# Kernel tuning notes

Measured on AMD Instinct MI355X. Metric: run time of the kernel, lower is better.

Reference implementation:

```python
import jax, jax.numpy as jnp
import numpy as np

C, CP, H, D, N, B = 128, 16, 8, 16, 2048, 1
INF = 1e8


def _ln(x, w=None, b=None, eps=1e-5):
    mu = jnp.mean(x, axis=-1, keepdims=True)
    var = jnp.var(x, axis=-1, keepdims=True)
    y = (x - mu) * jax.lax.rsqrt(var + eps)
    if w is not None:
        y = y * w
    if b is not None:
        y = y + b
    return y


def _ada_ln(a, s, sln_w, gw, gb, skw):
    # AdaLN: non-affine LN on a, weight-only LN on s, sigmoid gate + skip from s
    a = _ln(a)
    s = _ln(s, sln_w)
    return jax.nn.sigmoid(s @ gw + gb) * a + s @ skw


def _betas(n, n_keys=128, inf=INF):
    # centers at 16 + 32k; query row i belongs to window i//32, keys within +/- n_keys//2 of center
    i = jnp.arange(n)
    c = 16 + 32 * (i // 32)
    j = jnp.arange(n)
    ok = (j[None, :] >= (c - n_keys // 2)[:, None]) & (j[None, :] < (c + n_keys // 2)[:, None])
    return jnp.where(ok, 0.0, -inf).astype(jnp.float32)


def _forward(atom_single, atom_proj, atom_pair, mask,
             a_sln_w, a_gate_w, a_gate_b, a_skip_w,
             wq, bq, wk, wv, wg, bg, wo, bo,
             lnz_w, lnz_b, wz, wog, bog,
             t_sln_w, t_gate_w, t_gate_b, t_skip_w,
             w_sw, w_hid, w_out, t_wog, t_bog):
    bs, n, _ = atom_single.shape
    betas = _betas(n)
    # ---- AttentionPairBias (input_gating=True, residual handled outside) ----
    a = _ada_ln(atom_single, atom_proj, a_sln_w, a_gate_w, a_gate_b, a_skip_w)
    q = (a @ wq + bq).reshape(bs, n, H, D)
    k = (a @ wk).reshape(bs, n, H, D)
    v = (a @ wv).reshape(bs, n, H, D)
    pair_bias = _ln(atom_pair, lnz_w, lnz_b) @ wz            # (bs, n, n, H)
    pair_bias = jnp.transpose(pair_bias, (0, 3, 1, 2)) + betas  # (bs, H, n, n)
    mask_bias = (INF * (mask - 1.0))[:, None, None, :]          # (bs, 1, 1, n)
    logits = jnp.einsum('bqhd,bkhd->bhqk', q, k) / np.float32(np.sqrt(D))
    logits = logits + pair_bias + mask_bias
    probs = jax.nn.softmax(logits, axis=-1)
    o = jnp.einsum('bhqk,bkhd->bqhd', probs, v)
    g = jax.nn.sigmoid(a @ wg + bg).reshape(bs, n, H, D)
    o = (o * g).reshape(bs, n, H * D) @ wo + bo
    o = jax.nn.sigmoid(atom_proj @ wog + bog) * o             # conditioned output gate
    atom_single = atom_single + o
    # ---- ConditionedTransitionBlock (SwiGLU, n=2) ----
    t = _ada_ln(atom_single, atom_proj, t_sln_w, t_gate_w, t_gate_b, t_skip_w)
    hidden = jax.nn.silu(t @ w_sw) * (t @ w_hid)              # (bs, n, 2C)
    t_out = jax.nn.sigmoid(atom_proj @ t_wog + t_bog) * (hidden @ w_out)
    return atom_single + t_out


def setup_inputs() -> dict:
    key = jax.random.key(0)
    ks = iter(jax.random.split(key, 40))
    rn = lambda shape, s=1.0: jax.random.normal(next(ks), shape, jnp.float32) * s
    p = 0.05
    return {
        "atom_single": rn((B, N, C)),
        "atom_proj": rn((B, N, C)),
        "atom_pair": rn((B, N, N, CP)),
        "mask": jnp.ones((B, N), jnp.float32),
        "a_sln_w": jnp.ones((C,), jnp.float32), "a_gate_w": rn((C, C), p), "a_gate_b": jnp.zeros((C,), jnp.float32), "a_skip_w": rn((C, C), p),
        "wq": rn((C, C), p), "bq": jnp.zeros((C,), jnp.float32),
        "wk": rn((C, C), p), "wv": rn((C, C), p),
        "wg": rn((C, C), p), "bg": jnp.ones((C,), jnp.float32),
        "wo": rn((C, C), p), "bo": jnp.zeros((C,), jnp.float32),
        "lnz_w": jnp.ones((CP,), jnp.float32), "lnz_b": jnp.zeros((CP,), jnp.float32), "wz": rn((CP, H), p),
        "wog": rn((C, C), p), "bog": jnp.full((C,), -2.0, jnp.float32),
        "t_sln_w": jnp.ones((C,), jnp.float32), "t_gate_w": rn((C, C), p), "t_gate_b": jnp.zeros((C,), jnp.float32), "t_skip_w": rn((C, C), p),
        "w_sw": rn((C, 2 * C), p), "w_hid": rn((C, 2 * C), p), "w_out": rn((2 * C, C), p),
        "t_wog": rn((C, C), p), "t_bog": jnp.full((C,), -2.0, jnp.float32),
    }


def reference(atom_single, atom_proj, atom_pair, mask,
              a_sln_w, a_gate_w, a_gate_b, a_skip_w,
              wq, bq, wk, wv, wg, bg, wo, bo,
              lnz_w, lnz_b, wz, wog, bog,
              t_sln_w, t_gate_w, t_gate_b, t_skip_w,
              w_sw, w_hid, w_out, t_wog, t_bog):
    out = _forward(atom_single, atom_proj, atom_pair, mask,
                   a_sln_w, a_gate_w, a_gate_b, a_skip_w,
                   wq, bq, wk, wv, wg, bg, wo, bo,
                   lnz_w, lnz_b, wz, wog, bog,
                   t_sln_w, t_gate_w, t_gate_b, t_skip_w,
                   w_sw, w_hid, w_out, t_wog, t_bog)
    return (out, atom_proj, atom_pair)
```

## Files before the change

### kernel.cpp

```cpp
#include <hip/hip_runtime.h>
#include <math.h>

#define NN 2048
#define CC 128
#define HH 8
#define DD 16
#define NKEY 128
#define INFV 1e8f
#define NPR ((long)NN * CC / 4)
#define NCPTOT (NPR + (long)NN * NN * 4)
#define SLOT 2176
#define ANP 36
#define ASLOT 1152

__device__ __forceinline__ float sigm(float x) { return 1.f / (1.f + expf(-x)); }

struct Args {
  const float *atom_single, *atom_proj, *atom_pair, *mask;
  const float *a_sln_w, *a_gate_w, *a_gate_b, *a_skip_w;
  const float *wq, *bq, *wk, *wv, *wg, *bg, *wo, *bo;
  const float *lnz_w, *lnz_b, *wz, *wog, *bog;
  const float *t_sln_w, *t_gate_w, *t_gate_b, *t_skip_w;
  const float *w_sw, *w_hid, *w_out, *t_wog, *t_bog;
  float *out;
  float *s_ln_a, *s_ln_t, *ln_as, *a_mat, *qm, *km, *vm, *gm, *ogm,
        *single2, *t_mat, *hidden, *bias;
  long cut[9];
};

__device__ __forceinline__ void copy_span(const Args& a, int s, long rb, long nb, int tid) {
  long c0 = a.cut[s], c1 = a.cut[s + 1];
  const float4* proj4 = (const float4*)a.atom_proj;
  const float4* pair4 = (const float4*)a.atom_pair;
  float4* dst = (float4*)(a.out + (long)NN * CC);
  long stride = nb * 256;
  long i = c0 + rb * 256 + tid;
  for (; i + 3 * stride < c1; i += 4 * stride) {
    long i1 = i + stride, i2 = i + 2 * stride, i3 = i + 3 * stride;
    float4 x0 = (i  < NPR) ? proj4[i]  : pair4[i  - NPR];
    float4 x1 = (i1 < NPR) ? proj4[i1] : pair4[i1 - NPR];
    float4 x2 = (i2 < NPR) ? proj4[i2] : pair4[i2 - NPR];
    float4 x3 = (i3 < NPR) ? proj4[i3] : pair4[i3 - NPR];
    dst[i] = x0; dst[i1] = x1; dst[i2] = x2; dst[i3] = x3;
  }
  for (; i < c1; i += stride) dst[i] = (i < NPR) ? proj4[i] : pair4[i - NPR];
}

__device__ __forceinline__ void gsingle_pf(float* sm, int tid,
    const float* __restrict__ A1, const float* __restrict__ B1, int lda1, int ldb1, int K1,
    int r0, int c0, float acc1[4][4]) {
  float* buf0 = sm;
  float* buf1 = sm + 2 * SLOT;
  int tr = (tid >> 4) * 4, tc = (tid & 15) * 4;
  int ar = tid >> 5, ak = tid & 31;
  int bk = tid >> 6, bc = tid & 63;
  float pA[2][8], pB[2][8];
  auto LD = [&](int kb, int s) {
#pragma unroll
    for (int j = 0; j < 8; ++j) {
      pA[s][j] = A1[(long)(r0 + ar + 8 * j) * lda1 + kb + ak];
      pB[s][j] = B1[(long)(kb + bk + 4 * j) * ldb1 + c0 + bc];
    }
  };
  auto WR = [&](float* buf, int s) {
    float* B1s_ = buf + SLOT;
#pragma unroll
    for (int j = 0; j < 8; ++j) {
      buf[ak * 68 + ar + 8 * j] = pA[s][j];
      B1s_[(bk + 4 * j) * 68 + bc] = pB[s][j];
    }
  };
  auto CMP = [&](float* cur) {
    float* As_ = cur;
    float* B1s_ = cur + SLOT;
#pragma unroll 4
    for (int k = 0; k < 32; ++k) {
      float4 a1 = *(const float4*)&As_[k * 68 + tr];
      float4 b1 = *(const float4*)&B1s_[k * 68 + tc];
      float a1v[4] = {a1.x, a1.y, a1.z, a1.w};
      float b1v[4] = {b1.x, b1.y, b1.z, b1.w};
#pragma unroll
      for (int i = 0; i < 4; ++i)
#pragma unroll
        for (int j = 0; j < 4; ++j) acc1[i][j] = fmaf(a1v[i], b1v[j], acc1[i][j]);
    }
  };
  int nk = K1 / 32;
  LD(0, 0);
  if (nk > 1) LD(32, 1);
  WR(buf0, 0);
  __syncthreads();
  for (int kt = 0; kt < nk; kt += 2) {
    if (kt + 2 < nk) LD((kt + 2) * 32, 0);
    if (kt + 1 < nk) WR(buf1, 1);
    CMP(buf0);
    __syncthreads();
    if (kt + 1 >= nk) break;
    if (kt + 3 < nk) LD((kt + 3) * 32, 1);
    if (kt + 2 < nk) WR(buf0, 0);
    CMP(buf1);
    __syncthreads();
  }
}

template <bool SHA>
__device__ __forceinline__ void gdual32(float* sm, int tid,
    const float* __restrict__ A1, const float* __restrict__ B1, int lda1, int ldb1, int K1,
    const float* __restrict__ A2, const float* __restrict__ B2, int lda2, int ldb2, int K2,
    int r0, int c0, float acc1[2][4], float acc2[2][4]) {
  const int offB1 = ASLOT;
  const int offA2 = ASLOT + SLOT;
  const int offB2 = SHA ? (ASLOT + SLOT) : (2 * ASLOT + SLOT);
  const int bufsz = SHA ? (ASLOT + 2 * SLOT) : (2 * ASLOT + 2 * SLOT);
  float* buf0 = sm;
  float* buf1 = sm + bufsz;
  int tr2 = (tid >> 4) * 2, tc4 = (tid & 15) * 4;
  int ar = tid & 31, ak4 = (tid >> 5) * 4;
  int bk = tid >> 6, bc = tid & 63;
  float4 vA1[2], vA2[2];
  float pB1[2][8], pB2[2][8];

  auto LD = [&](int kb, int s, bool twof) {
    vA1[s] = *(const float4*)&A1[(long)(r0 + ar) * lda1 + kb + ak4];
#pragma unroll
    for (int j = 0; j < 8; ++j)
      pB1[s][j] = B1[(long)(kb + bk + 4 * j) * ldb1 + c0 + bc];
    if (twof) {
      if constexpr (!SHA) vA2[s] = *(const float4*)&A2[(long)(r0 + ar) * lda2 + kb + ak4];
#pragma unroll
      for (int j = 0; j < 8; ++j)
        pB2[s][j] = B2[(long)(kb + bk + 4 * j) * ldb2 + c0 + bc];
    }
  };
  auto WR = [&](float* buf, int s, bool twof) {
    float* As_ = buf;
    float* B1s_ = buf + offB1;
    As_[(ak4 + 0) * ANP + ar] = vA1[s].x;
    As_[(ak4 + 1) * ANP + ar] = vA1[s].y;
    As_[(ak4 + 2) * ANP + ar] = vA1[s].z;
    As_[(ak4 + 3) * ANP + ar] = vA1[s].w;
#pragma unroll
    for (int j = 0; j < 8; ++j) B1s_[(bk + 4 * j) * 68 + bc] = pB1[s][j];
    if (twof) {
      float* B2s_ = buf + offB2;
      if constexpr (!SHA) {
        float* A2s_ = buf + offA2;
        A2s_[(ak4 + 0) * ANP + ar] = vA2[s].x;
        A2s_[(ak4 + 1) * ANP + ar] = vA2[s].y;
        A2s_[(ak4 + 2) * ANP + ar] = vA2[s].z;
        A2s_[(ak4 + 3) * ANP + ar] = vA2[s].w;
      }
#pragma unroll
      for (int j = 0; j < 8; ++j) B2s_[(bk + 4 * j) * 68 + bc] = pB2[s][j];
    }
  };
  auto CMP = [&](float* cur, bool twoc) {
    float* As_ = cur;
    float* B1s_ = cur + offB1;
    float* A2s_ = cur + offA2;
    float* B2s_ = cur + offB2;
    if (twoc) {
#pragma unroll 4
      for (int k = 0; k < 32; ++k) {
        float2 a1 = *(const float2*)&As_[k * ANP + tr2];
        float4 b1 = *(const float4*)&B1s_[k * 68 + tc4];
        float4 b2 = *(const float4*)&B2s_[k * 68 + tc4];
        float2 a2;
        if constexpr (SHA) a2 = a1; else a2 = *(const float2*)&A2s_[k * ANP + tr2];
        float a1v[2] = {a1.x, a1.y};
        float a2v[2] = {a2.x, a2.y};
        float b1v[4] = {b1.x, b1.y, b1.z, b1.w};
        float b2v[4] = {b2.x, b2.y, b2.z, b2.w};
#pragma unroll
        for (int i = 0; i < 2; ++i)
#pragma unroll
          for (int j = 0; j < 4; ++j) {
            acc1[i][j] = fmaf(a1v[i], b1v[j], acc1[i][j]);
            acc2[i][j] = fmaf(a2v[i], b2v[j], acc2[i][j]);
          }
      }
    } else {
#pragma unroll 4
      for (int k = 0; k < 32; ++k) {
        float2 a1 = *(const float2*)&As_[k * ANP + tr2];
        float4 b1 = *(const float4*)&B1s_[k * 68 + tc4];
        float a1v[2] = {a1.x, a1.y};
        float b1v[4] = {b1.x, b1.y, b1.z, b1.w};
#pragma unroll
        for (int i = 0; i < 2; ++i)
#pragma unroll
          for (int j = 0; j < 4; ++j) acc1[i][j] = fmaf(a1v[i], b1v[j], acc1[i][j]);
      }
    }
  };

  int nk = K1 / 32;
  LD(0, 0, 0 < K2);
  if (nk > 1) LD(32, 1, 32 < K2);
  WR(buf0, 0, 0 < K2);
  __syncthreads();
  for (int kt = 0; kt < nk; kt += 2) {
    if (kt + 2 < nk) LD((kt + 2) * 32, 0, (kt + 2) * 32 < K2);
    if (kt + 1 < nk) WR(buf1, 1, (kt + 1) * 32 < K2);
    CMP(buf0, kt * 32 < K2);
    __syncthreads();
    if (kt + 1 >= nk) break;
    if (kt + 3 < nk) LD((kt + 3) * 32, 1, (kt + 3) * 32 < K2);
    if (kt + 2 < nk) WR(buf0, 0, (kt + 2) * 32 < K2);
    CMP(buf1, (kt + 1) * 32 < K2);
    __syncthreads();
  }
}

__device__ __forceinline__ void bias_stage(const Args& a, long lo, long hi,
                                           int bid, int nb, int tid, float* sm) {
  float* swz = sm;
  float* swn = sm + 128;
  float* sbn = sm + 144;
  if (tid < 128) swz[tid] = a.wz[tid];
  else if (tid < 144) swn[tid - 128] = a.lnz_w[tid - 128];
  else if (tid < 160) sbn[tid - 144] = a.lnz_b[tid - 144];
  __syncthreads();
  for (long e = lo + bid * 256 + tid; e < hi; e += (long)nb * 256) {
    int q = (int)(e >> 7), kk = (int)(e & 127);
    int k = (q >> 5) * 32 - 48 + kk;
    float o[HH];
    if (k >= 0 && k < NN) {
      const float4* p = (const float4*)(a.atom_pair + ((long)q * NN + k) * 16);
      float4 x0 = p[0], x1 = p[1], x2 = p[2], x3 = p[3];
      float x[16] = {x0.x, x0.y, x0.z, x0.w, x1.x, x1.y, x1.z, x1.w,
                     x2.x, x2.y, x2.z, x2.w, x3.x, x3.y, x3.z, x3.w};
      float s = 0.f, ss = 0.f;
#pragma unroll
      for (int c = 0; c < 16; ++c) { s += x[c]; ss += x[c] * x[c]; }
      float mu = s * (1.f / 16.f);
      float r = rsqrtf(ss * (1.f / 16.f) - mu * mu + 1e-5f);
#pragma unroll
      for (int h = 0; h < HH; ++h) o[h] = 0.f;
#pragma unroll
      for (int c = 0; c < 16; ++c) {
        float y = (x[c] - mu) * r * swn[c] + sbn[c];
#pragma unroll
        for (int h = 0; h < HH; ++h) o[h] = fmaf(y, swz[c * HH + h], o[h]);
      }
      float mb = INFV * (a.mask[k] - 1.f);
#pragma unroll
      for (int h = 0; h < HH; ++h) o[h] += mb;
    } else {
#pragma unroll
      for (int h = 0; h < HH; ++h) o[h] = -INFV;
    }
#pragma unroll
    for (int h = 0; h < HH; ++h) a.bias[(long)h * NN * NKEY + e] = o[h];
  }
}

__device__ __forceinline__ void ln1_stage(const Args& a, int lb, int tid) {
  int base = lb * 64;
  int lane = tid & 63;
  for (int r = base + (tid >> 6); r < base + 64; r += 4) {
    {
      float2 v = *(const float2*)(a.atom_single + (long)r * CC + lane * 2);
      float s = v.x + v.y, ss = v.x * v.x + v.y * v.y;
#pragma unroll
      for (int m = 1; m < 64; m <<= 1) { s += __shfl_xor(s, m); ss += __shfl_xor(ss, m); }
      float mu = s * (1.f / CC);
      float rr = rsqrtf(ss * (1.f / CC) - mu * mu + 1e-5f);
      *(float2*)(a.ln_as + (long)r * CC + lane * 2) =
          make_float2((v.x - mu) * rr, (v.y - mu) * rr);
    }
    {
      float2 v = *(const float2*)(a.atom_proj + (long)r * CC + lane * 2);
      float s = v.x + v.y, ss = v.x * v.x + v.y * v.y;
#pragma unroll
      for (int m = 1; m < 64; m <<= 1) { s += __shfl_xor(s, m); ss += __shfl_xor(ss, m); }
      float mu = s * (1.f / CC);
      float rr = rsqrtf(ss * (1.f / CC) - mu * mu + 1e-5f);
      float y0 = (v.x - mu) * rr, y1 = (v.y - mu) * rr;
      float2 wa = *(const float2*)(a.a_sln_w + lane * 2);
      float2 wt = *(const float2*)(a.t_sln_w + lane * 2);
      *(float2*)(a.s_ln_a + (long)r * CC + lane * 2) = make_float2(y0 * wa.x, y1 * wa.y);
      *(float2*)(a.s_ln_t + (long)r * CC + lane * 2) = make_float2(y0 * wt.x, y1 * wt.y);
    }
  }
}

template <bool INLN>
__device__ __forceinline__ void adaln32_stage(const Args& a, const float* A, const float* gw,
                                              const float* gb, const float* skw,
                                              const float* lnm_or_src, float* outp,
                                              int bid, int tid, float* sm, float* sst) {
  int r0 = (bid & 63) * 32, c0 = (bid >> 6) * 64;
  if constexpr (INLN) {
    int row = tid >> 3, cg = (tid & 7) * 16;
    const float* src = lnm_or_src + (long)(r0 + row) * CC + cg;
    float s = 0.f, ss = 0.f;
#pragma unroll
    for (int j = 0; j < 4; ++j) {
      float4 v = *(const float4*)(src + j * 4);
      s += v.x + v.y + v.z + v.w;
      ss += v.x * v.x + v.y * v.y + v.z * v.z + v.w * v.w;
    }
#pragma unroll
    for (int m = 1; m < 8; m <<= 1) { s += __shfl_xor(s, m); ss += __shfl_xor(ss, m); }
    if ((tid & 7) == 0) {
      float mu = s * (1.f / CC);
      sst[2 * row] = mu;
      sst[2 * row + 1] = rsqrtf(ss * (1.f / CC) - mu * mu + 1e-5f);
    }
  }
  float acc1[2][4] = {{0}}, acc2[2][4] = {{0}};
  gdual32<true>(sm, tid, A, gw, 128, 128, 128, A, skw, 128, 128, 128, r0, c0, acc1, acc2);
  int tr2 = (tid >> 4) * 2, tc4 = (tid & 15) * 4;
#pragma unroll
  for (int i = 0; i < 2; ++i) {
    long r = r0 + tr2 + i;
    float lv[4];
    if constexpr (INLN) {
      float mu = sst[2 * (tr2 + i)], rr = sst[2 * (tr2 + i) + 1];
      float4 sv = *(const float4*)(lnm_or_src + r * CC + c0 + tc4);
      lv[0] = (sv.x - mu) * rr; lv[1] = (sv.y - mu) * rr;
      lv[2] = (sv.z - mu) * rr; lv[3] = (sv.w - mu) * rr;
    } else {
      float4 lm = *(const float4*)(lnm_or_src + r * CC + c0 + tc4);
      lv[0] = lm.x; lv[1] = lm.y; lv[2] = lm.z; lv[3] = lm.w;
    }
    float o[4];
#pragma unroll
    for (int j = 0; j < 4; ++j)
      o[j] = sigm(acc1[i][j] + gb[c0 + tc4 + j]) * lv[j] + acc2[i][j];
    *(float4*)(outp + r * CC + c0 + tc4) = make_float4(o[0], o[1], o[2], o[3]);
  }
}

__device__ __forceinline__ void gemm4_stage(const Args& a, int bid, int tid, float* sm) {
  int r0 = (bid & 31) * 64;
  int cg4 = (bid >> 5) * 64;
  int mat = cg4 >> 7;
  int c0 = cg4 & 127;
  const float* B = (mat == 0) ? a.wq : (mat == 1) ? a.wk : (mat == 2) ? a.wv : a.wg;
  float acc[4][4] = {{0}};
  gsingle_pf(sm, tid, a.a_mat, B, 128, 128, 128, r0, c0, acc);
  float* outp = (mat == 0) ? a.qm : (mat == 1) ? a.km : (mat == 2) ? a.vm : a.gm;
  int tr = (tid >> 4) * 4, tc = (tid & 15) * 4;
#pragma unroll
  for (int i = 0; i < 4; ++i) {
    long r = r0 + tr + i;
    float o[4];
#pragma unroll
    for (int j = 0; j < 4; ++j) {
      float x = acc[i][j];
      if (mat == 0) x += a.bq[c0 + tc + j];
      if (mat == 3) x = sigm(x + a.bg[c0 + tc + j]);
      o[j] = x;
    }
    *(float4*)(outp + r * CC + c0 + tc) = make_float4(o[0], o[1], o[2], o[3]);
  }
}

__device__ __forceinline__ void attn_unit(const Args& a, int u, int tid, float* sm) {
  int w = u & 63, h = u >> 6;
  int q0 = w * 32, k0 = w * 32 - 48;
  float* Qs = sm;
  float* Ks = sm + 544;
  float* Vs = sm + 3104;
  float* Ps = sm + 5664;
  for (int i = tid; i < 32 * 16; i += 256) {
    int qi = i >> 4, d = i & 15;
    Qs[qi * 17 + d] = a.qm[(long)(q0 + qi) * CC + h * DD + d];
  }
  for (int i = tid; i < 128 * 16; i += 256) {
    int kk = i >> 4, d = i & 15;
    int k = k0 + kk;
    bool ok = (k >= 0 && k < NN);
    Ks[kk * 20 + d] = ok ? a.km[(long)k * CC + h * DD + d] : 0.f;
    Vs[kk * 20 + d] = ok ? a.vm[(long)k * CC + h * DD + d] : 0.f;
  }
  __syncthreads();
  int qi = tid >> 3, kg = tid & 7;
  const float* brow = a.bias + (long)h * NN * NKEY + (long)(q0 + qi) * NKEY;
  float qreg[16];
#pragma unroll
  for (int d = 0; d < 16; ++d) qreg[d] = Qs[qi * 17 + d];
  float l[16];
#pragma unroll
  for (int j = 0; j < 16; ++j) {
    int kk = kg + 8 * j;
    const float4* kr = (const float4*)&Ks[kk * 20];
    float4 k0v = kr[0], k1v = kr[1], k2v = kr[2], k3v = kr[3];
    float acc = 0.f;
    acc = fmaf(qreg[0], k0v.x, acc);  acc = fmaf(qreg[1], k0v.y, acc);
    acc = fmaf(qreg[2], k0v.z, acc);  acc = fmaf(qreg[3], k0v.w, acc);
    acc = fmaf(qreg[4], k1v.x, acc);  acc = fmaf(qreg[5], k1v.y, acc);
    acc = fmaf(qreg[6], k1v.z, acc);  acc = fmaf(qreg[7], k1v.w, acc);
    acc = fmaf(qreg[8], k2v.x, acc);  acc = fmaf(qreg[9], k2v.y, acc);
    acc = fmaf(qreg[10], k2v.z, acc); acc = fmaf(qreg[11], k2v.w, acc);
    acc = fmaf(qreg[12], k3v.x, acc); acc = fmaf(qreg[13], k3v.y, acc);
    acc = fmaf(qreg[14], k3v.z, acc); acc = fmaf(qreg[15], k3v.w, acc);
    l[j] = acc * 0.25f + brow[kk];
  }
  float m = l[0];
#pragma unroll
  for (int j = 1; j < 16; ++j) m = fmaxf(m, l[j]);
#pragma unroll
  for (int mm = 1; mm < 8; mm <<= 1) m = fmaxf(m, __shfl_xor(m, mm));
  float sum = 0.f;
#pragma unroll
  for (int j = 0; j < 16; ++j) { l[j] = expf(l[j] - m); sum += l[j]; }
#pragma unroll
  for (int mm = 1; mm < 8; mm <<= 1) sum += __shfl_xor(sum, mm);
  float inv = 1.f / sum;
#pragma unroll
  for (int j = 0; j < 16; ++j) Ps[qi * 132 + kg + 8 * j] = l[j] * inv;
  __syncthreads();
  int d0 = tid & 7;
  float o0 = 0.f, o1 = 0.f;
#pragma unroll 8
  for (int kk = 0; kk < 128; ++kk) {
    float p = Ps[qi * 132 + kk];
    o0 = fmaf(p, Vs[kk * 20 + d0], o0);
    o1 = fmaf(p, Vs[kk * 20 + d0 + 8], o1);
  }
  long base = (long)(q0 + qi) * CC + h * DD;
  a.ogm[base + d0] = o0 * a.gm[base + d0];
  a.ogm[base + d0 + 8] = o1 * a.gm[base + d0 + 8];
}

__device__ __forceinline__ void out1_32(const Args& a, int bid, int tid, float* sm) {
  int r0 = (bid & 63) * 32, c0 = (bid >> 6) * 64;
  float accX[2][4] = {{0}}, accW[2][4] = {{0}};
  gdual32<false>(sm, tid, a.ogm, a.wo, 128, 128, 128, a.atom_proj, a.wog, 128, 128, 128,
                 r0, c0, accX, accW);
  int tr2 = (tid >> 4) * 2, tc4 = (tid & 15) * 4;
#pragma unroll
  for (int i = 0; i < 2; ++i) {
    long r = r0 + tr2 + i;
    float4 sv = *(const float4*)(a.atom_single + r * CC + c0 + tc4);
    float s[4] = {sv.x, sv.y, sv.z, sv.w};
    float o[4];
#pragma unroll
    for (int j = 0; j < 4; ++j) {
      int c = c0 + tc4 + j;
      o[j] = s[j] + sigm(accW[i][j] + a.bog[c]) * (accX[i][j] + a.bo[c]);
    }
    *(float4*)(a.single2 + r * CC + c0 + tc4) = make_float4(o[0], o[1], o[2], o[3]);
  }
}

__device__ __forceinline__ void swiglu_32(const Args& a, int bid, int tid, float* sm) {
  int r0 = (bid & 63) * 32, c0 = (bid >> 6) * 64;
  float acc1[2][4] = {{0}}, acc2[2][4] = {{0}};
  gdual32<true>(sm, tid, a.t_mat, a.w_sw, 128, 256, 128, a.t_mat, a.w_hid, 128, 256, 128,
                r0, c0, acc1, acc2);
  int tr2 = (tid >> 4) * 2, tc4 = (tid & 15) * 4;
#pragma unroll
  for (int i = 0; i < 2; ++i) {
    long r = r0 + tr2 + i;
    float o[4];
#pragma unroll
    for (int j = 0; j < 4; ++j) {
      float x = acc1[i][j];
      o[j] = x * sigm(x) * acc2[i][j];
    }
    *(float4*)(a.hidden + r * 256 + c0 + tc4) = make_float4(o[0], o[1], o[2], o[3]);
  }
}

__device__ __forceinline__ void out2_32(const Args& a, int bid, int tid, float* sm) {
  int r0 = (bid & 63) * 32, c0 = (bid >> 6) * 64;
  float accX[2][4] = {{0}}, accW[2][4] = {{0}};
  gdual32<false>(sm, tid, a.hidden, a.w_out, 256, 128, 256, a.atom_proj, a.t_wog, 128, 128, 128,
                 r0, c0, accX, accW);
  int tr2 = (tid >> 4) * 2, tc4 = (tid & 15) * 4;
#pragma unroll
  for (int i = 0; i < 2; ++i) {
    long r = r0 + tr2 + i;
    float4 sv = *(const float4*)(a.single2 + r * CC + c0 + tc4);
    float s[4] = {sv.x, sv.y, sv.z, sv.w};
    float o[4];
#pragma unroll
    for (int j = 0; j < 4; ++j) {
      int c = c0 + tc4 + j;
      o[j] = s[j] + sigm(accW[i][j] + a.t_bog[c]) * accX[i][j];
    }
    *(float4*)(a.out + r * CC + c0 + tc4) = make_float4(o[0], o[1], o[2], o[3]);
  }
}

#define BIAS_TOT ((long)NN * NKEY)
#define BIAS_1 (BIAS_TOT / 3)
#define BIAS_2 (2 * BIAS_TOT / 3)

__global__ __launch_bounds__(256) void k_head(Args a) {
  __shared__ __align__(16) float sm[160];
  int bid = blockIdx.x, tid = threadIdx.x;
  if (bid < 96) bias_stage(a, 0, BIAS_1, bid, 96, tid, sm);
  else if (bid < 128) ln1_stage(a, bid - 96, tid);
  else copy_span(a, 0, bid - 128, gridDim.x - 128, tid);
}

__global__ __launch_bounds__(256) void k_adaln_a(Args a) {
  __shared__ __align__(16) float sm[2 * (ASLOT + 2 * SLOT) + 64];
  int bid = blockIdx.x, tid = threadIdx.x;
  if (bid < 128)
    adaln32_stage<false>(a, a.s_ln_a, a.a_gate_w, a.a_gate_b, a.a_skip_w, a.ln_as, a.a_mat,
                         bid, tid, sm, nullptr);
  else if (bid < 224) bias_stage(a, BIAS_1, BIAS_2, bid - 128, 96, tid, sm);
  else copy_span(a, 1, bid - 224, gridDim.x - 224, tid);
}

__global__ __launch_bounds__(256) void k_qkvg(Args a) {
  __shared__ __align__(16) float sm[2 * 2 * SLOT];
  int bid = blockIdx.x, tid = threadIdx.x;
  if (bid < 256) gemm4_stage(a, bid, tid, sm);
  else if (bid < 352) bias_stage(a, BIAS_2, BIAS_TOT, bid - 256, 96, tid, sm);
  else copy_span(a, 2, bid - 352, gridDim.x - 352, tid);
}

__global__ __launch_bounds__(256) void k_attn(Args a) {
  __shared__ __align__(16) float sm[9888];
  int bid = blockIdx.x, tid = threadIdx.x;
  if (bid < 512) attn_unit(a, bid, tid, sm);
  else copy_span(a, 3, bid - 512, gridDim.x - 512, tid);
}

__global__ __launch_bounds__(256) void k_out1(Args a) {
  __shared__ __align__(16) float sm[2 * (2 * ASLOT + 2 * SLOT)];
  int bid = blockIdx.x, tid = threadIdx.x;
  if (bid < 128) out1_32(a, bid, tid, sm);
  else copy_span(a, 4, bid - 128, gridDim.x - 128, tid);
}

__global__ __launch_bounds__(256) void k_adaln_t(Args a) {
  __shared__ __align__(16) float sm[2 * (ASLOT + 2 * SLOT) + 64];
  int bid = blockIdx.x, tid = threadIdx.x;
  if (bid < 128)
    adaln32_stage<true>(a, a.s_ln_t, a.t_gate_w, a.t_gate_b, a.t_skip_w, a.single2, a.t_mat,
                        bid, tid, sm, sm + 2 * (ASLOT + 2 * SLOT));
  else copy_span(a, 5, bid - 128, gridDim.x - 128, tid);
}

__global__ __launch_bounds__(256) void k_swiglu(Args a) {
  __shared__ __align__(16) float sm[2 * (ASLOT + 2 * SLOT)];
  int bid = blockIdx.x, tid = threadIdx.x;
  if (bid < 256) swiglu_32(a, bid, tid, sm);
  else copy_span(a, 6, bid - 256, gridDim.x - 256, tid);
}

__global__ __launch_bounds__(256) void k_out2(Args a) {
  __shared__ __align__(16) float sm[2 * (2 * ASLOT + 2 * SLOT)];
  int bid = blockIdx.x, tid = threadIdx.x;
  if (bid < 128) out2_32(a, bid, tid, sm);
  else copy_span(a, 7, bid - 128, gridDim.x - 128, tid);
}

extern "C" void kernel_launch(void* const* d_in, const int* in_sizes, int n_in,
                              void* d_out, int out_size, void* d_ws, size_t ws_size,
                              hipStream_t stream) {
  (void)in_sizes; (void)n_in; (void)out_size; (void)ws_size;
  Args a;
  a.atom_single = (const float*)d_in[0];
  a.atom_proj   = (const float*)d_in[1];
  a.atom_pair   = (const float*)d_in[2];
  a.mask        = (const float*)d_in[3];
  a.a_sln_w  = (const float*)d_in[4];
  a.a_gate_w = (const float*)d_in[5];
  a.a_gate_b = (const float*)d_in[6];
  a.a_skip_w = (const float*)d_in[7];
  a.wq = (const float*)d_in[8];  a.bq = (const float*)d_in[9];
  a.wk = (const float*)d_in[10]; a.wv = (const float*)d_in[11];
  a.wg = (const float*)d_in[12]; a.bg = (const float*)d_in[13];
  a.wo = (const float*)d_in[14]; a.bo = (const float*)d_in[15];
  a.lnz_w = (const float*)d_in[16]; a.lnz_b = (const float*)d_in[17];
  a.wz = (const float*)d_in[18];
  a.wog = (const float*)d_in[19]; a.bog = (const float*)d_in[20];
  a.t_sln_w  = (const float*)d_in[21];
  a.t_gate_w = (const float*)d_in[22];
  a.t_gate_b = (const float*)d_in[23];
  a.t_skip_w = (const float*)d_in[24];
  a.w_sw  = (const float*)d_in[25];
  a.w_hid = (const float*)d_in[26];
  a.w_out = (const float*)d_in[27];
  a.t_wog = (const float*)d_in[28];
  a.t_bog = (const float*)d_in[29];
  a.out = (float*)d_out;

  float* ws = (float*)d_ws;
  const long NC = (long)NN * CC;
  a.s_ln_a  = ws + 0 * NC;
  a.s_ln_t  = ws + 1 * NC;
  a.ln_as   = ws + 2 * NC;
  a.a_mat   = ws + 3 * NC;
  a.qm      = ws + 4 * NC;
  a.km      = ws + 5 * NC;
  a.vm      = ws + 6 * NC;
  a.gm      = ws + 7 * NC;
  a.ogm     = ws + 8 * NC;
  a.single2 = ws + 9 * NC;
  a.t_mat   = ws + 11 * NC;
  a.hidden  = ws + 12 * NC;
  a.bias    = ws + 14 * NC;

  const int cum[9] = {0, 9, 17, 24, 32, 40, 48, 56, 64};
  for (int i = 0; i < 9; ++i) a.cut[i] = NCPTOT * (long)cum[i] / 64;

  k_head   <<<2048, 256, 0, stream>>>(a);
  k_adaln_a<<<2048, 256, 0, stream>>>(a);
  k_qkvg   <<<2048, 256, 0, stream>>>(a);
  k_attn   <<<2048, 256, 0, stream>>>(a);
  k_out1   <<<2048, 256, 0, stream>>>(a);
  k_adaln_t<<<2048, 256, 0, stream>>>(a);
  k_swiglu <<<2048, 256, 0, stream>>>(a);
  k_out2   <<<2048, 256, 0, stream>>>(a);
}
```

Before: 156.7 us.

## Use atomic work-stealing for passthrough copies and nontemporal loads/stores

The passthrough copy of atom_proj and atom_pair into the output was statically split across leftover blocks in each stage kernel. Now every block, including compute blocks once they finish their stage work, takes chunks of the copy from a per-stage atomic counter, so copy work follows whichever blocks free up. The copy also uses nontemporal loads and stores to keep streaming data out of the caches. The cost is atomic traffic and extra barriers per chunk. There is also a counter-reset ordering risk: counters are zeroed in k_head and first used in the next kernel, which the stream ordering covers.

```diff
diff --git a/kernel.cpp b/kernel.cpp
--- a/kernel.cpp
+++ b/kernel.cpp
@@ -12,6 +12,9 @@
 #define SLOT 2176
 #define ANP 36
 #define ASLOT 1152
+#define CHUNK4 2048L
+
+typedef float f4 __attribute__((ext_vector_type(4)));
 
 __device__ __forceinline__ float sigm(float x) { return 1.f / (1.f + expf(-x)); }
 
@@ -25,25 +28,59 @@
   float *out;
   float *s_ln_a, *s_ln_t, *ln_as, *a_mat, *qm, *km, *vm, *gm, *ogm,
         *single2, *t_mat, *hidden, *bias;
+  unsigned* cnt;
   long cut[9];
 };
 
 __device__ __forceinline__ void copy_span(const Args& a, int s, long rb, long nb, int tid) {
   long c0 = a.cut[s], c1 = a.cut[s + 1];
-  const float4* proj4 = (const float4*)a.atom_proj;
-  const float4* pair4 = (const float4*)a.atom_pair;
-  float4* dst = (float4*)(a.out + (long)NN * CC);
+  const f4* proj4 = (const f4*)a.atom_proj;
+  const f4* pair4 = (const f4*)a.atom_pair;
+  f4* dst = (f4*)(a.out + (long)NN * CC);
   long stride = nb * 256;
   long i = c0 + rb * 256 + tid;
   for (; i + 3 * stride < c1; i += 4 * stride) {
     long i1 = i + stride, i2 = i + 2 * stride, i3 = i + 3 * stride;
-    float4 x0 = (i  < NPR) ? proj4[i]  : pair4[i  - NPR];
-    float4 x1 = (i1 < NPR) ? proj4[i1] : pair4[i1 - NPR];
-    float4 x2 = (i2 < NPR) ? proj4[i2] : pair4[i2 - NPR];
-    float4 x3 = (i3 < NPR) ? proj4[i3] : pair4[i3 - NPR];
-    dst[i] = x0; dst[i1] = x1; dst[i2] = x2; dst[i3] = x3;
-  }
-  for (; i < c1; i += stride) dst[i] = (i < NPR) ? proj4[i] : pair4[i - NPR];
+    f4 x0 = (i  < NPR) ? __builtin_nontemporal_load(&proj4[i])
+                       : __builtin_nontemporal_load(&pair4[i - NPR]);
+    f4 x1 = (i1 < NPR) ? __builtin_nontemporal_load(&proj4[i1])
+                       : __builtin_nontemporal_load(&pair4[i1 - NPR]);
+    f4 x2 = (i2 < NPR) ? __builtin_nontemporal_load(&proj4[i2])
+                       : __builtin_nontemporal_load(&pair4[i2 - NPR]);
+    f4 x3 = (i3 < NPR) ? __builtin_nontemporal_load(&proj4[i3])
+                       : __builtin_nontemporal_load(&pair4[i3 - NPR]);
+    __builtin_nontemporal_store(x0, &dst[i]);
+    __builtin_nontemporal_store(x1, &dst[i1]);
+    __builtin_nontemporal_store(x2, &dst[i2]);
+    __builtin_nontemporal_store(x3, &dst[i3]);
+  }
+  for (; i < c1; i += stride) {
+    f4 v = (i < NPR) ? __builtin_nontemporal_load(&proj4[i])
+                     : __builtin_nontemporal_load(&pair4[i - NPR]);
+    __builtin_nontemporal_store(v, &dst[i]);
+  }
+}
+
+__device__ void copy_steal(const Args& a, int s, int tid) {
+  __shared__ unsigned sticket;
+  long c0 = a.cut[s], c1 = a.cut[s + 1];
+  const f4* proj4 = (const f4*)a.atom_proj;
+  const f4* pair4 = (const f4*)a.atom_pair;
+  f4* dst = (f4*)(a.out + (long)NN * CC);
+  unsigned* cnt = a.cnt + s;
+  while (true) {
+    __syncthreads();
+    if (tid == 0) sticket = atomicAdd(cnt, 1u);
+    __syncthreads();
+    long base = c0 + (long)sticket * CHUNK4;
+    if (base >= c1) break;
+    long end = (base + CHUNK4 < c1) ? base + CHUNK4 : c1;
+    for (long i = base + tid; i < end; i += 256) {
+      f4 v = (i < NPR) ? __builtin_nontemporal_load(&proj4[i])
+                       : __builtin_nontemporal_load(&pair4[i - NPR]);
+      __builtin_nontemporal_store(v, &dst[i]);
+    }
+  }
 }
 
 __device__ __forceinline__ void gsingle_pf(float* sm, int tid,
@@ -494,6 +531,7 @@
 __global__ __launch_bounds__(256) void k_head(Args a) {
   __shared__ __align__(16) float sm[160];
   int bid = blockIdx.x, tid = threadIdx.x;
+  if (bid == 0 && tid < 8) a.cnt[tid] = 0;
   if (bid < 96) bias_stage(a, 0, BIAS_1, bid, 96, tid, sm);
   else if (bid < 128) ln1_stage(a, bid - 96, tid);
   else copy_span(a, 0, bid - 128, gridDim.x - 128, tid);
@@ -506,7 +544,7 @@
     adaln32_stage<false>(a, a.s_ln_a, a.a_gate_w, a.a_gate_b, a.a_skip_w, a.ln_as, a.a_mat,
                          bid, tid, sm, nullptr);
   else if (bid < 224) bias_stage(a, BIAS_1, BIAS_2, bid - 128, 96, tid, sm);
-  else copy_span(a, 1, bid - 224, gridDim.x - 224, tid);
+  copy_steal(a, 1, tid);
 }
 
 __global__ __launch_bounds__(256) void k_qkvg(Args a) {
@@ -514,21 +552,21 @@
   int bid = blockIdx.x, tid = threadIdx.x;
   if (bid < 256) gemm4_stage(a, bid, tid, sm);
   else if (bid < 352) bias_stage(a, BIAS_2, BIAS_TOT, bid - 256, 96, tid, sm);
-  else copy_span(a, 2, bid - 352, gridDim.x - 352, tid);
+  copy_steal(a, 2, tid);
 }
 
 __global__ __launch_bounds__(256) void k_attn(Args a) {
   __shared__ __align__(16) float sm[9888];
   int bid = blockIdx.x, tid = threadIdx.x;
   if (bid < 512) attn_unit(a, bid, tid, sm);
-  else copy_span(a, 3, bid - 512, gridDim.x - 512, tid);
+  copy_steal(a, 3, tid);
 }
 
 __global__ __launch_bounds__(256) void k_out1(Args a) {
   __shared__ __align__(16) float sm[2 * (2 * ASLOT + 2 * SLOT)];
   int bid = blockIdx.x, tid = threadIdx.x;
   if (bid < 128) out1_32(a, bid, tid, sm);
-  else copy_span(a, 4, bid - 128, gridDim.x - 128, tid);
+  copy_steal(a, 4, tid);
 }
 
 __global__ __launch_bounds__(256) void k_adaln_t(Args a) {
@@ -537,21 +575,21 @@
   if (bid < 128)
     adaln32_stage<true>(a, a.s_ln_t, a.t_gate_w, a.t_gate_b, a.t_skip_w, a.single2, a.t_mat,
                         bid, tid, sm, sm + 2 * (ASLOT + 2 * SLOT));
-  else copy_span(a, 5, bid - 128, gridDim.x - 128, tid);
+  copy_steal(a, 5, tid);
 }
 
 __global__ __launch_bounds__(256) void k_swiglu(Args a) {
   __shared__ __align__(16) float sm[2 * (ASLOT + 2 * SLOT)];
   int bid = blockIdx.x, tid = threadIdx.x;
   if (bid < 256) swiglu_32(a, bid, tid, sm);
-  else copy_span(a, 6, bid - 256, gridDim.x - 256, tid);
+  copy_steal(a, 6, tid);
 }
 
 __global__ __launch_bounds__(256) void k_out2(Args a) {
   __shared__ __align__(16) float sm[2 * (2 * ASLOT + 2 * SLOT)];
   int bid = blockIdx.x, tid = threadIdx.x;
   if (bid < 128) out2_32(a, bid, tid, sm);
-  else copy_span(a, 7, bid - 128, gridDim.x - 128, tid);
+  copy_steal(a, 7, tid);
 }
 
 extern "C" void kernel_launch(void* const* d_in, const int* in_sizes, int n_in,
@@ -600,6 +638,7 @@
   a.t_mat   = ws + 11 * NC;
   a.hidden  = ws + 12 * NC;
   a.bias    = ws + 14 * NC;
+  a.cnt     = (unsigned*)(ws + 22 * NC);
 
   const int cum[9] = {0, 9, 17, 24, 32, 40, 48, 56, 64};
   for (int i = 0; i < 9; ++i) a.cut[i] = NCPTOT * (long)cum[i] / 64;
```

Result: slower. 319.1 us (+103.6%).
